# Kernel tuning notes

Hardware: AMD Instinct MI355X
Metric: run time of the kernel (lower is better)

The kernel has to match this reference:

```python
import jax, jax.numpy as jnp
import numpy as np

NUM_JOINTS = 21
BN_EPS = 1e-5


def hand_adjacency():
    J = NUM_JOINTS
    a = np.zeros((J, J), dtype=np.float32)
    # wrist to finger bases
    for j in (1, 5, 9, 13, 17):
        a[0, j] = a[j, 0] = 1
    # finger chains
    for base in (1, 5, 9, 13, 17):
        for i in range(base, base + 3):
            a[i, i + 1] = a[i + 1, i] = 1
    a += np.eye(J, dtype=np.float32)
    d = a.sum(axis=1)
    dinv = np.power(d, -0.5)
    dinv[np.isinf(dinv)] = 0.0
    D = np.diag(dinv)
    return (D @ a @ D).astype(np.float32)


def setup_inputs() -> dict:
    key = jax.random.key(0)
    ks = jax.random.split(key, 16)
    S, B, HD = 256, 128, 42
    IN, HID = 2, 64
    x = jax.random.normal(ks[0], (S, B, HD), dtype=jnp.float32)
    # xavier-uniform weights
    lim1 = float(np.sqrt(6.0 / (IN + HID)))
    lim2 = float(np.sqrt(6.0 / (HID + IN)))
    W1 = jax.random.uniform(ks[1], (IN, HID), minval=-lim1, maxval=lim1, dtype=jnp.float32)
    b1 = jnp.zeros((HID,), dtype=jnp.float32)
    W2 = jax.random.uniform(ks[2], (HID, IN), minval=-lim2, maxval=lim2, dtype=jnp.float32)
    b2 = jnp.zeros((IN,), dtype=jnp.float32)
    # BatchNorm (eval mode): affine params + running stats
    g1 = 1.0 + 0.1 * jax.random.normal(ks[3], (HID,), dtype=jnp.float32)
    be1 = 0.1 * jax.random.normal(ks[4], (HID,), dtype=jnp.float32)
    m1 = 0.1 * jax.random.normal(ks[5], (HID,), dtype=jnp.float32)
    v1 = 0.5 + jax.random.uniform(ks[6], (HID,), dtype=jnp.float32)
    g2 = 1.0 + 0.1 * jax.random.normal(ks[7], (IN,), dtype=jnp.float32)
    be2 = 0.1 * jax.random.normal(ks[8], (IN,), dtype=jnp.float32)
    m2 = 0.1 * jax.random.normal(ks[9], (IN,), dtype=jnp.float32)
    v2 = 0.5 + jax.random.uniform(ks[10], (IN,), dtype=jnp.float32)
    adj = jnp.asarray(hand_adjacency())
    return {"x": x, "adj": adj, "W1": W1, "b1": b1, "W2": W2, "b2": b2,
            "g1": g1, "be1": be1, "m1": m1, "v1": v1,
            "g2": g2, "be2": be2, "m2": m2, "v2": v2}


def _gcn_bn(h, adj, W, b, g, be, m, v, act):
    # h: (S, B, J, Cin) -> (S, B, J, Cout)
    s = jnp.einsum('sbjc,cd->sbjd', h, W)          # feature transform
    o = jnp.einsum('ij,sbjd->sbid', adj, s) + b    # joint aggregation + bias
    o = (o - m) * (g * jax.lax.rsqrt(v + BN_EPS)) + be  # BN eval, per-channel
    return jax.nn.relu(o) if act else o


def reference(x, adj, W1, b1, W2, b2, g1, be1, m1, v1, g2, be2, m2, v2):
    S, B, HD = x.shape
    C = HD // NUM_JOINTS
    h = x.reshape(S, B, NUM_JOINTS, C)
    h = _gcn_bn(h, adj, W1, b1, g1, be1, m1, v1, act=True)   # dropout is identity in eval
    h = _gcn_bn(h, adj, W2, b2, g2, be2, m2, v2, act=False)
    return h.reshape(S, B, HD) + x
```

## Files before the change

### kernel.cpp

```cpp
#include <hip/hip_runtime.h>

typedef float f2 __attribute__((ext_vector_type(2)));

#define NJ 21

#define W00 0.16666667f
#define W0B 0.23570226f
#define W33 0.33333333f
#define WMT 0.40824829f
#define WTT 0.5f

template<int PAT>
__device__ __forceinline__ float dpp_add(float v) {
    int r = __builtin_amdgcn_update_dpp(0, __float_as_int(v), PAT, 0xF, 0xF, true);
    return v + __int_as_float(r);
}

__device__ __forceinline__ void aggregate(const f2* __restrict__ s, f2* __restrict__ d) {
    d[0] = W00 * s[0] + W0B * (s[1] + s[5] + s[9] + s[13] + s[17]);
#pragma unroll
    for (int f = 1; f <= 17; f += 4) {
        d[f]     = W0B * s[0] + W33 * (s[f] + s[f + 1]);
        d[f + 1] = W33 * (s[f] + s[f + 1] + s[f + 2]);
        d[f + 2] = W33 * (s[f + 1] + s[f + 2]) + WMT * s[f + 3];
        d[f + 3] = WMT * s[f + 2] + WTT * s[f + 3];
    }
}

__global__ __launch_bounds__(256) void hgcn_kernel(
    const float* __restrict__ x,
    const float* __restrict__ adj,
    const float* __restrict__ W1,
    const float* __restrict__ b1,
    const float* __restrict__ W2,
    const float* __restrict__ b2,
    const float* __restrict__ g1,
    const float* __restrict__ be1,
    const float* __restrict__ m1,
    const float* __restrict__ v1,
    const float* __restrict__ g2,
    const float* __restrict__ be2,
    const float* __restrict__ m2,
    const float* __restrict__ v2,
    float* __restrict__ out)
{
    (void)adj;
    __shared__ float4 sc1[67];
    __shared__ float  sc2[64];
    __shared__ float  sD[2];

    const int tid = threadIdx.x;

    if (tid < 64) {
        const int d = tid;
        const float k1  = g1[d] * rsqrtf(v1[d] + 1e-5f);
        const float A   = W1[d]      * k1;
        const float B   = W1[64 + d] * k1;
        const float C   = (b1[d] - m1[d]) * k1 + be1[d];
        const float k20 = g2[0] * rsqrtf(v2[0] + 1e-5f);
        const float k21 = g2[1] * rsqrtf(v2[1] + 1e-5f);
        sc1[d + (d >> 4)] = make_float4(A, B, C, W2[2 * d] * k20);
        sc2[d] = W2[2 * d + 1] * k21;
        if (d < 2) {
            const float k2 = (d == 0) ? k20 : k21;
            sD[d] = (b2[d] - m2[d]) * k2 + be2[d];
        }
    }
    __syncthreads();

    const int gt = blockIdx.x * 256 + tid;
    const int t  = gt >> 2;
    const int q  = gt & 3;

    const float2* __restrict__ xin = (const float2*)x + (size_t)t * NJ;
    f2 h[NJ];
#pragma unroll
    for (int j = 0; j < NJ; ++j) {
        const float2 v = xin[j];
        h[j] = (f2){v.x, v.y};
    }

    f2 a[NJ + 1];
    aggregate(h, a);
    a[NJ] = (f2){0.f, 0.f};

    f2 ap0[11], ap1[11];
#pragma unroll
    for (int k = 0; k < 11; ++k) {
        ap0[k] = (f2){a[2 * k].x, a[2 * k + 1].x};
        ap1[k] = (f2){a[2 * k].y, a[2 * k + 1].y};
    }

    f2 s0[11], s1[11];
#pragma unroll
    for (int k = 0; k < 11; ++k) { s0[k] = (f2){0.f, 0.f}; s1[k] = (f2){0.f, 0.f}; }

    const int cbase = q * 17;
#pragma unroll
    for (int dd = 0; dd < 16; ++dd) {
        const float4 c  = sc1[cbase + dd];
        const float w21 = sc2[(q << 4) + dd];
#pragma unroll
        for (int k = 0; k < 11; ++k) {
            f2 v = ap0[k] * c.x + ap1[k] * c.y + c.z;
            v = __builtin_elementwise_max(v, (f2){0.f, 0.f});
            s0[k] += v * c.w;
            s1[k] += v * w21;
        }
    }

#pragma unroll
    for (int k = 0; k < 11; ++k) {
        s0[k].x = dpp_add<0xB1>(s0[k].x);  s0[k].x = dpp_add<0x4E>(s0[k].x);
        s0[k].y = dpp_add<0xB1>(s0[k].y);  s0[k].y = dpp_add<0x4E>(s0[k].y);
        s1[k].x = dpp_add<0xB1>(s1[k].x);  s1[k].x = dpp_add<0x4E>(s1[k].x);
        s1[k].y = dpp_add<0xB1>(s1[k].y);  s1[k].y = dpp_add<0x4E>(s1[k].y);
    }

    f2 vv[NJ], o[NJ];
#pragma unroll
    for (int j = 0; j < NJ; ++j) {
        vv[j].x = (j & 1) ? s0[j >> 1].y : s0[j >> 1].x;
        vv[j].y = (j & 1) ? s1[j >> 1].y : s1[j >> 1].x;
    }
    aggregate(vv, o);

    const f2 Dv = (f2){sD[0], sD[1]};
    const int lo = (q == 0) ? 0 : (q == 1) ? 5 : (q == 2) ? 11 : 16;
    const int hi = (q == 0) ? 5 : (q == 1) ? 11 : (q == 2) ? 16 : 21;

    float2* __restrict__ outw = (float2*)out + (size_t)t * NJ;
#pragma unroll
    for (int i = 0; i < NJ; ++i) {
        if (i >= lo && i < hi) {
            const f2 r = o[i] + Dv + h[i];
            float2 st; st.x = r.x; st.y = r.y;
            outw[i] = st;
        }
    }
}

extern "C" void kernel_launch(void* const* d_in, const int* in_sizes, int n_in,
                              void* d_out, int out_size, void* d_ws, size_t ws_size,
                              hipStream_t stream) {
    (void)in_sizes; (void)n_in; (void)d_ws; (void)ws_size; (void)out_size;
    const float* x   = (const float*)d_in[0];
    const float* adj = (const float*)d_in[1];
    const float* W1  = (const float*)d_in[2];
    const float* b1  = (const float*)d_in[3];
    const float* W2  = (const float*)d_in[4];
    const float* b2  = (const float*)d_in[5];
    const float* g1  = (const float*)d_in[6];
    const float* be1 = (const float*)d_in[7];
    const float* m1  = (const float*)d_in[8];
    const float* v1  = (const float*)d_in[9];
    const float* g2  = (const float*)d_in[10];
    const float* be2 = (const float*)d_in[11];
    const float* m2  = (const float*)d_in[12];
    const float* v2  = (const float*)d_in[13];

    hgcn_kernel<<<512, 256, 0, stream>>>(x, adj, W1, b1, W2, b2,
                                         g1, be1, m1, v1, g2, be2, m2, v2,
                                         (float*)d_out);
}
```

Before: 91.24 us.

## Stage input and output tiles through LDS for coalesced float4 global access

Each block now loads its 64-token slice of x into shared memory with fully coalesced float4 loads, and the per-token threads read from LDS instead of issuing strided float2 global loads. Outputs are written to a shared tile and then stored to global memory as coalesced float4 writes, with the bias and residual added at that point. The goal is to cut the cost of uncoalesced 168-byte-stride global accesses. In exchange it uses about 21 KB of LDS per block, which can lower occupancy, and adds a second barrier.

Result: no change. 89.61 us (-1.8%).

```diff
diff --git a/kernel.cpp b/kernel.cpp
--- a/kernel.cpp
+++ b/kernel.cpp
@@ -48,8 +48,18 @@
     __shared__ float4 sc1[67];
     __shared__ float  sc2[64];
     __shared__ float  sD[2];
+    __shared__ float  xs[64 * 42];
+    __shared__ float  os[64 * 42];
 
     const int tid = threadIdx.x;
+
+    const float4* __restrict__ xg =
+        (const float4*)(x + (size_t)blockIdx.x * (64 * 42));
+    float4* xs4 = (float4*)xs;
+    const float4 r0 = xg[tid];
+    const float4 r1 = xg[tid + 256];
+    float4 r2;
+    if (tid < 160) r2 = xg[tid + 512];
 
     if (tid < 64) {
         const int d = tid;
@@ -66,17 +76,20 @@
             sD[d] = (b2[d] - m2[d]) * k2 + be2[d];
         }
     }
+
+    xs4[tid]       = r0;
+    xs4[tid + 256] = r1;
+    if (tid < 160) xs4[tid + 512] = r2;
     __syncthreads();
 
-    const int gt = blockIdx.x * 256 + tid;
-    const int t  = gt >> 2;
-    const int q  = gt & 3;
+    const int tl = tid >> 2;
+    const int q  = tid & 3;
 
-    const float2* __restrict__ xin = (const float2*)x + (size_t)t * NJ;
+    const float2* __restrict__ xt = (const float2*)(xs + tl * 42);
     f2 h[NJ];
 #pragma unroll
     for (int j = 0; j < NJ; ++j) {
-        const float2 v = xin[j];
+        const float2 v = xt[j];
         h[j] = (f2){v.x, v.y};
     }
 
@@ -125,18 +138,32 @@
     }
     aggregate(vv, o);
 
-    const f2 Dv = (f2){sD[0], sD[1]};
     const int lo = (q == 0) ? 0 : (q == 1) ? 5 : (q == 2) ? 11 : 16;
     const int hi = (q == 0) ? 5 : (q == 1) ? 11 : (q == 2) ? 16 : 21;
-
-    float2* __restrict__ outw = (float2*)out + (size_t)t * NJ;
+    float2* __restrict__ ot = (float2*)(os + tl * 42);
 #pragma unroll
     for (int i = 0; i < NJ; ++i) {
         if (i >= lo && i < hi) {
-            const f2 r = o[i] + Dv + h[i];
-            float2 st; st.x = r.x; st.y = r.y;
-            outw[i] = st;
+            float2 st; st.x = o[i].x; st.y = o[i].y;
+            ot[i] = st;
         }
+    }
+    __syncthreads();
+
+    const float4 Df = make_float4(sD[0], sD[1], sD[0], sD[1]);
+    float4* __restrict__ og = (float4*)(out + (size_t)blockIdx.x * (64 * 42));
+    const float4* os4 = (const float4*)os;
+
+    float4 o0 = os4[tid],       x0 = xs4[tid];
+    float4 o1 = os4[tid + 256], x1 = xs4[tid + 256];
+    og[tid] = make_float4(o0.x + x0.x + Df.x, o0.y + x0.y + Df.y,
+                          o0.z + x0.z + Df.z, o0.w + x0.w + Df.w);
+    og[tid + 256] = make_float4(o1.x + x1.x + Df.x, o1.y + x1.y + Df.y,
+                                o1.z + x1.z + Df.z, o1.w + x1.w + Df.w);
+    if (tid < 160) {
+        float4 o2 = os4[tid + 512], x2 = xs4[tid + 512];
+        og[tid + 512] = make_float4(o2.x + x2.x + Df.x, o2.y + x2.y + Df.y,
+                                    o2.z + x2.z + Df.z, o2.w + x2.w + Df.w);
     }
 }
 
```
